# Kernel tuning notes

Hardware: AMD Instinct MI355X
Metric: run time of the kernel (lower is better)

The kernel has to match this reference:

```python
import jax, jax.numpy as jnp
import numpy as np

HIDDEN, HEADS, HDIM = 1024, 8, 64
B, S = 4, 8192
LN_EPS = 1e-6


def setup_inputs() -> dict:
    key = jax.random.key(0)
    ks = jax.random.split(key, 12)
    inner = HEADS * HDIM
    sd = HIDDEN ** -0.5
    return {
        "x": jax.random.normal(ks[0], (B, S, HIDDEN), jnp.float32),
        "Wq": jax.random.normal(ks[1], (HIDDEN, inner), jnp.float32) * sd,
        "bq": jnp.zeros((inner,), jnp.float32),
        "Wk": jax.random.normal(ks[2], (HIDDEN, inner), jnp.float32) * sd,
        "bk": jnp.zeros((inner,), jnp.float32),
        "Wv": jax.random.normal(ks[3], (HIDDEN, inner), jnp.float32) * sd,
        "bv": jnp.zeros((inner,), jnp.float32),
        "Wo": jax.random.normal(ks[4], (inner, HIDDEN), jnp.float32) * (inner ** -0.5),
        "bo": jnp.zeros((HIDDEN,), jnp.float32),
        "alpha": jnp.ones((HEADS, HDIM), jnp.float32),
        "aug_param": jax.random.normal(ks[5], (1, HEADS, HDIM), jnp.float32),
        "ln_scale": jnp.ones((HIDDEN,), jnp.float32),
        "ln_bias": jnp.zeros((HIDDEN,), jnp.float32),
    }


def reference(x, Wq, bq, Wk, bk, Wv, bv, Wo, bo, alpha, aug_param, ln_scale, ln_bias):
    b, s, _ = x.shape
    h, d = alpha.shape
    scale = d ** -0.5
    q = (x @ Wq + bq).reshape(b, s, h, d)
    k = (x @ Wk + bk).reshape(b, s, h, d)
    v = (x @ Wv + bv).reshape(b, s, h, d)
    decay = jax.nn.sigmoid(alpha)  # (h, d)

    def step(state, qkv):
        q_t, k_t, v_t = qkv  # each (b, h, d)
        attn = jax.nn.softmax(jnp.einsum('bhd,bhd->bh', q_t, k_t) * scale, axis=-1)
        new_state = decay * state + (1.0 - decay) * attn[..., None] * v_t
        return new_state, new_state

    qs = jnp.moveaxis(q, 1, 0)  # (s, b, h, d)
    ks_ = jnp.moveaxis(k, 1, 0)
    vs = jnp.moveaxis(v, 1, 0)
    init = jnp.zeros((b, h, d), x.dtype)
    _, states = jax.lax.scan(step, init, (qs, ks_, vs))
    states = jnp.moveaxis(states, 0, 1)  # (b, s, h, d)

    aug = jax.nn.sigmoid(q * aug_param)  # aug_param (1,h,d) broadcasts over (b,s,h,d)
    out = (q * states + aug).reshape(b, s, h * d)
    out = out @ Wo + bo
    mean = jnp.mean(out, axis=-1, keepdims=True)
    var = jnp.var(out, axis=-1, keepdims=True)
    return (out - mean) * jax.lax.rsqrt(var + LN_EPS) * ln_scale + ln_bias
```

## Files before the change

### kernel.cpp

```cpp
#include <hip/hip_runtime.h>
#include <hip/hip_bf16.h>


#define HIDDEN 1024
#define HEADS 8
#define HDIM 64
#define INNER 512
#define BATCH 4
#define SEQ 8192
#define ROWS (BATCH*SEQ)
#define NCHUNK 128
#define CHLEN 64

typedef unsigned short u16;
typedef unsigned int u32;
typedef __attribute__((ext_vector_type(8))) short bf16x8;
typedef __attribute__((ext_vector_type(4))) float f32x4;

__device__ __forceinline__ float b2f(u16 u) { return __uint_as_float(((u32)u) << 16); }
__device__ __forceinline__ u16 f2b(float f) {
  u32 u = __float_as_uint(f);
  u32 r = u + 0x7fffu + ((u >> 16) & 1u);
  return (u16)(r >> 16);
}
__device__ __forceinline__ u32 pack2(float a, float b) {
  return (u32)f2b(a) | ((u32)f2b(b) << 16);
}

#define GLOAD_LDS16(gp, lp)                                                  \
  __builtin_amdgcn_global_load_lds(                                          \
      (const __attribute__((address_space(1))) u32*)(gp),                    \
      (__attribute__((address_space(3))) u32*)(lp), 16, 0, 0)

__global__ __launch_bounds__(256) void prep_xw(
    const float* __restrict__ x, u16* __restrict__ xb,
    const float* __restrict__ Wq, const float* __restrict__ Wk,
    const float* __restrict__ Wv, const float* __restrict__ Wo,
    const float* __restrict__ bq, const float* __restrict__ bk,
    const float* __restrict__ bv,
    u16* __restrict__ Wt, u16* __restrict__ Wot, float* __restrict__ bcat) {
  const int b = blockIdx.x;
  if (b < 16384) {
    size_t i = ((size_t)b * 256 + threadIdx.x) * 8;
    float4 a = *(const float4*)(x + i);
    float4 c = *(const float4*)(x + i + 4);
    uint4 w = {pack2(a.x, a.y), pack2(a.z, a.w), pack2(c.x, c.y), pack2(c.z, c.w)};
    *(uint4*)(xb + i) = w;
  } else {
    const int WELEM = HIDDEN * INNER;
    int idx = (b - 16384) * 256 + threadIdx.x;
    if (idx < 3 * WELEM) {
      int z = idx / WELEM;
      int rem = idx - z * WELEM;
      int n = rem >> 10;
      int k = rem & 1023;
      const float* W = (z == 0) ? Wq : (z == 1) ? Wk : Wv;
      Wt[idx] = f2b(W[k * INNER + n]);
    } else {
      int rem = idx - 3 * WELEM;
      int n = rem >> 9;
      int k = rem & 511;
      Wot[rem] = f2b(Wo[k * HIDDEN + n]);
    }
    if (idx < 3 * INNER) {
      int z = idx >> 9;
      int n = idx & 511;
      bcat[idx] = (z == 0) ? bq[n] : (z == 1) ? bk[n] : bv[n];
    }
  }
}

__global__ __launch_bounds__(256) void prep_w(
    const float* __restrict__ Wq, const float* __restrict__ Wk,
    const float* __restrict__ Wv, const float* __restrict__ Wo,
    const float* __restrict__ bq, const float* __restrict__ bk,
    const float* __restrict__ bv,
    u16* __restrict__ Wt, u16* __restrict__ Wot, float* __restrict__ bcat) {
  const int WELEM = HIDDEN * INNER;
  int idx = blockIdx.x * 256 + threadIdx.x;
  if (idx < 3 * WELEM) {
    int z = idx / WELEM;
    int rem = idx - z * WELEM;
    int n = rem >> 10;
    int k = rem & 1023;
    const float* W = (z == 0) ? Wq : (z == 1) ? Wk : Wv;
    Wt[idx] = f2b(W[k * INNER + n]);
  } else {
    int rem = idx - 3 * WELEM;
    int n = rem >> 9;
    int k = rem & 511;
    Wot[rem] = f2b(Wo[k * HIDDEN + n]);
  }
  if (idx < 3 * INNER) {
    int z = idx >> 9;
    int n = idx & 511;
    bcat[idx] = (z == 0) ? bq[n] : (z == 1) ? bk[n] : bv[n];
  }
}

template <int K, bool SPLIT3>
__global__ __launch_bounds__(512, 2) void gemm_rp(
    const u16* __restrict__ A, const u16* __restrict__ Bt,
    const float* __restrict__ bias,
    void* __restrict__ out0, void* __restrict__ out1, void* __restrict__ out2,
    int nTilesN) {
  constexpr int NT = K / 32;
  __shared__ u16 lds[4][16384];

  const int nwg = gridDim.x;
  const int chunk = nwg >> 3;
  const int bid = blockIdx.x;
  const int lin = (bid & 7) * chunk + (bid >> 3);
  const int nt = lin % nTilesN;
  const int mt = lin / nTilesN;
  const int m0 = mt * 256, n0 = nt * 256;
  const int N = nTilesN * 256;

  const int tid = threadIdx.x;
  const int lane = tid & 63;
  const int w = tid >> 6;
  const int wm = w >> 2;
  const int wn = w & 3;
  const int r16 = lane & 15, kq = lane >> 4;

  const int rt = tid >> 2;
  const int cg = (((tid & 3) << 3)) ^ (((rt >> 1) & 3) << 3);
  const u16* Ag = A + (size_t)(m0 + rt) * K + cg;
  const u16* Bg = Bt + (size_t)(n0 + rt) * K + cg;
  const int ldst = w * 512;

#define STAGE_AB(slot, kt)                                                    \
  {                                                                           \
    GLOAD_LDS16(Ag + (size_t)(kt) * 32, &lds[slot][ldst]);                    \
    GLOAD_LDS16(Ag + (size_t)(kt) * 32 + (size_t)128 * K,                     \
                &lds[slot][4096 + ldst]);                                     \
    GLOAD_LDS16(Bg + (size_t)(kt) * 32, &lds[slot][8192 + ldst]);             \
    GLOAD_LDS16(Bg + (size_t)(kt) * 32 + (size_t)128 * K,                     \
                &lds[slot][12288 + ldst]);                                    \
  }

  const int xk = (kq << 3) ^ (((r16 >> 1) & 3) << 3);
  const int aO = (wm * 128 + r16) * 32 + xk;
  const int bO = 8192 + (wn * 64 + r16) * 32 + xk;

  f32x4 acc[8][4] = {};
  bf16x8 r0_a[8], r0_b[4], r1_a[8], r1_b[4];

#define DSREAD(da, db, slot)                                                   \
  {                                                                            \
    const u16* sl = &lds[slot][0];                                             \
    _Pragma("unroll") for (int i = 0; i < 8; i++)                              \
        da[i] = *(const bf16x8*)&sl[aO + i * 512];                             \
    _Pragma("unroll") for (int j = 0; j < 4; j++)                              \
        db[j] = *(const bf16x8*)&sl[bO + j * 512];                             \
  }

#define MFMA_SET(sa, sb)                                                       \
  {                                                                            \
    __builtin_amdgcn_s_setprio(1);                                             \
    _Pragma("unroll") for (int i = 0; i < 8; i++)                              \
        _Pragma("unroll") for (int j = 0; j < 4; j++)                          \
            acc[i][j] = __builtin_amdgcn_mfma_f32_16x16x32_bf16(               \
                sa[i], sb[j], acc[i][j], 0, 0, 0);                             \
    __builtin_amdgcn_s_setprio(0);                                             \
  }

#define MFMA_RD(sa, sb, da, db, slot)                                          \
  {                                                                            \
    const u16* sl = &lds[slot][0];                                             \
    __builtin_amdgcn_s_setprio(1);                                             \
    _Pragma("unroll") for (int j = 0; j < 4; j++)                              \
        db[j] = *(const bf16x8*)&sl[bO + j * 512];                             \
    _Pragma("unroll") for (int i = 0; i < 8; i++) {                            \
      da[i] = *(const bf16x8*)&sl[aO + i * 512];                               \
      _Pragma("unroll") for (int j = 0; j < 4; j++)                            \
          acc[i][j] = __builtin_amdgcn_mfma_f32_16x16x32_bf16(                 \
              sa[i], sb[j], acc[i][j], 0, 0, 0);                               \
    }                                                                          \
    __builtin_amdgcn_s_setprio(0);                                             \
    __builtin_amdgcn_sched_group_barrier(0x100, 4, 0);        \
    _Pragma("unroll") for (int i = 0; i < 8; i++) {                            \
      __builtin_amdgcn_sched_group_barrier(0x100, 1, 0);      \
      __builtin_amdgcn_sched_group_barrier(0x8, 4, 0);             \
    }                                                                          \
  }

#define SYNCB                                                                  \
  {                                                                            \
    __builtin_amdgcn_sched_barrier(0);                                         \
    __builtin_amdgcn_s_barrier();                                              \
    __builtin_amdgcn_sched_barrier(0);                                         \
  }

#define VM4 asm volatile("s_waitcnt vmcnt(4)" ::: "memory")
#define VM0 asm volatile("s_waitcnt vmcnt(0)" ::: "memory")

  STAGE_AB(0, 0);
  STAGE_AB(1, 1);
  STAGE_AB(2, 2);
  VM4;
  SYNCB;
  DSREAD(r0_a, r0_b, 0);

  for (int t = 0; t + 6 <= NT; t += 2) {
    STAGE_AB((t + 3) & 3, t + 3);
    MFMA_RD(r0_a, r0_b, r1_a, r1_b, (t + 1) & 3);
    VM4;
    SYNCB;
    STAGE_AB((t + 4) & 3, t + 4);
    MFMA_RD(r1_a, r1_b, r0_a, r0_b, (t + 2) & 3);
    VM4;
    SYNCB;
  }
  STAGE_AB((NT - 1) & 3, NT - 1);
  MFMA_RD(r0_a, r0_b, r1_a, r1_b, (NT - 3) & 3);
  VM4;
  SYNCB;
  MFMA_RD(r1_a, r1_b, r0_a, r0_b, (NT - 2) & 3);
  VM0;
  SYNCB;
  MFMA_RD(r0_a, r0_b, r1_a, r1_b, (NT - 1) & 3);
  MFMA_SET(r1_a, r1_b);
  SYNCB;
#undef DSREAD
#undef MFMA_SET
#undef MFMA_RD
#undef SYNCB
#undef VM4
#undef VM0
#undef STAGE_AB

  float* fl = (float*)(&lds[0][0]) + w * 4096;
  const int zsel = SPLIT3 ? ((n0 + wn * 64) >> 9) : 0;
  u16* ob = SPLIT3 ? (u16*)((zsel == 0) ? out0 : (zsel == 1) ? out1 : out2)
                   : (u16*)out0;
  const int OC = SPLIT3 ? INNER : N;
  const int colloc = (lane & 7) * 8;
  const int gcol = (SPLIT3 ? ((n0 + wn * 64) & 511) : (n0 + wn * 64)) + colloc;
  const int lrowr = lane >> 3;
  float bvj[4];
#pragma unroll
  for (int j = 0; j < 4; j++) bvj[j] = bias[n0 + wn * 64 + j * 16 + r16];

#pragma unroll
  for (int pass = 0; pass < 4; ++pass) {
#pragma unroll
    for (int ii = 0; ii < 2; ++ii) {
#pragma unroll
      for (int j = 0; j < 4; ++j) {
#pragma unroll
        for (int q = 0; q < 4; ++q)
          fl[(ii * 16 + kq * 4 + q) * 68 + j * 16 + r16] =
              acc[pass * 2 + ii][j][q] + bvj[j];
      }
    }
#pragma unroll
    for (int inst = 0; inst < 4; ++inst) {
      int lr = inst * 8 + lrowr;
      float4 f0 = *(float4*)&fl[lr * 68 + colloc];
      float4 f1 = *(float4*)&fl[lr * 68 + colloc + 4];
      uint4 wv = {pack2(f0.x, f0.y), pack2(f0.z, f0.w),
                  pack2(f1.x, f1.y), pack2(f1.z, f1.w)};
      size_t grow = (size_t)(m0 + wm * 128 + pass * 32 + lr);
      *(uint4*)&ob[grow * OC + gcol] = wv;
    }
  }
}

template <bool A_BF16>
__global__ __launch_bounds__(256) void gemm128(
    const void* __restrict__ Aany, const u16* __restrict__ BtBase,
    const float* __restrict__ bias0, const float* __restrict__ bias1,
    const float* __restrict__ bias2,
    void* __restrict__ out0, void* __restrict__ out1, void* __restrict__ out2,
    int K) {
  __shared__ u16 As[128 * 32];
  __shared__ u16 Bs[128 * 32];
  const int N = gridDim.x * 128;
  const int z = blockIdx.z;
  const u16* Bt = BtBase + (size_t)z * N * K;
  const float* bias = (z == 0) ? bias0 : (z == 1) ? bias1 : bias2;
  void* Out = (z == 0) ? out0 : (z == 1) ? out1 : out2;
  const int tid = threadIdx.x;
  const int m0 = blockIdx.y * 128;
  const int n0 = blockIdx.x * 128;
  const int lane = tid & 63;
  const int wid = tid >> 6;
  const int wm = wid >> 1, wn = wid & 1;
  const int r16 = lane & 15, kq = lane >> 4;
  const int r = tid >> 1;
  const int half = tid & 1;
  f32x4 acc[4][4] = {};
  for (int k0 = 0; k0 < K; k0 += 32) {
    __syncthreads();
    if (A_BF16) {
      const u16* Ab = (const u16*)Aany;
      const int4* src = (const int4*)(Ab + (size_t)(m0 + r) * K + k0 + half * 16);
      int4 v0 = src[0];
      int4 v1 = src[1];
      *(int4*)&As[r * 32 + half * 16] = v0;
      *(int4*)&As[r * 32 + half * 16 + 8] = v1;
    } else {
      const float* Af = (const float*)Aany;
      const float4* src = (const float4*)(Af + (size_t)(m0 + r) * K + k0 + half * 16);
      float4 f0 = src[0], f1 = src[1], f2 = src[2], f3 = src[3];
      uint4 w0 = {pack2(f0.x, f0.y), pack2(f0.z, f0.w), pack2(f1.x, f1.y), pack2(f1.z, f1.w)};
      uint4 w1 = {pack2(f2.x, f2.y), pack2(f2.z, f2.w), pack2(f3.x, f3.y), pack2(f3.z, f3.w)};
      *(uint4*)&As[r * 32 + half * 16] = w0;
      *(uint4*)&As[r * 32 + half * 16 + 8] = w1;
    }
    {
      const int4* src = (const int4*)(Bt + (size_t)(n0 + r) * K + k0 + half * 16);
      int4 v0 = src[0];
      int4 v1 = src[1];
      *(int4*)&Bs[r * 32 + half * 16] = v0;
      *(int4*)&Bs[r * 32 + half * 16 + 8] = v1;
    }
    __syncthreads();
    bf16x8 a[4], b[4];
#pragma unroll
    for (int i = 0; i < 4; i++)
      a[i] = *(const bf16x8*)&As[(wm * 64 + i * 16 + r16) * 32 + kq * 8];
#pragma unroll
    for (int j = 0; j < 4; j++)
      b[j] = *(const bf16x8*)&Bs[(wn * 64 + j * 16 + r16) * 32 + kq * 8];
#pragma unroll
    for (int i = 0; i < 4; i++)
#pragma unroll
      for (int j = 0; j < 4; j++)
        acc[i][j] = __builtin_amdgcn_mfma_f32_16x16x32_bf16(a[i], b[j], acc[i][j], 0, 0, 0);
  }
#pragma unroll
  for (int j = 0; j < 4; j++) {
    int col = n0 + wn * 64 + j * 16 + r16;
    float bv = bias[col];
#pragma unroll
    for (int i = 0; i < 4; i++) {
#pragma unroll
      for (int q = 0; q < 4; q++) {
        int row = m0 + wm * 64 + i * 16 + kq * 4 + q;
        float v = acc[i][j][q] + bv;
        ((u16*)Out)[(size_t)row * N + col] = f2b(v);
      }
    }
  }
}

__global__ __launch_bounds__(256) void attn_kernel(
    const u16* __restrict__ qb, const u16* __restrict__ kb,
    float* __restrict__ attn) {
  int lane = threadIdx.x & 63;
  int wid = threadIdx.x >> 6;
  size_t t = (size_t)blockIdx.x * 4 + wid;
  int4 qv = *(const int4*)(qb + t * INNER + lane * 8);
  int4 kv = *(const int4*)(kb + t * INNER + lane * 8);
  const u16* qu = (const u16*)&qv;
  const u16* ku = (const u16*)&kv;
  float s = 0.f;
#pragma unroll
  for (int j = 0; j < 8; j++) s += b2f(qu[j]) * b2f(ku[j]);
  s += __shfl_xor(s, 1);
  s += __shfl_xor(s, 2);
  s += __shfl_xor(s, 4);
  s *= 0.125f;
  float mx = s;
  mx = fmaxf(mx, __shfl_xor(mx, 8));
  mx = fmaxf(mx, __shfl_xor(mx, 16));
  mx = fmaxf(mx, __shfl_xor(mx, 32));
  float e = __expf(s - mx);
  float sm = e;
  sm += __shfl_xor(sm, 8);
  sm += __shfl_xor(sm, 16);
  sm += __shfl_xor(sm, 32);
  float a = e / sm;
  if ((lane & 7) == 0) attn[t * HEADS + (lane >> 3)] = a;
}

__global__ __launch_bounds__(512) void scan_phase1(
    const u16* __restrict__ vb, const float* __restrict__ attn,
    const float* __restrict__ alpha, float* __restrict__ ends) {
  int hd = threadIdx.x;
  int h = hd >> 6;
  int c = blockIdx.x, b = blockIdx.y;
  float decay = 1.f / (1.f + __expf(-alpha[hd]));
  float om = 1.f - decay;
  size_t base = (size_t)b * SEQ + (size_t)c * CHLEN;
  float st = 0.f;
#pragma unroll 8
  for (int i = 0; i < CHLEN; i++) {
    size_t t = base + i;
    float a = attn[t * HEADS + h];
    float v = b2f(vb[t * INNER + hd]);
    st = decay * st + om * a * v;
  }
  ends[((size_t)b * NCHUNK + c) * INNER + hd] = st;
}

__global__ __launch_bounds__(512) void scan_phase2(
    const float* __restrict__ ends, const float* __restrict__ alpha,
    float* __restrict__ carries) {
  int hd = threadIdx.x;
  int b = blockIdx.x;
  float decay = 1.f / (1.f + __expf(-alpha[hd]));
  float dL = __powf(decay, (float)CHLEN);
  float carry = 0.f;
#pragma unroll 8
  for (int c = 0; c < NCHUNK; c++) {
    size_t idx = ((size_t)b * NCHUNK + c) * INNER + hd;
    carries[idx] = carry;
    carry = dL * carry + ends[idx];
  }
}

__global__ __launch_bounds__(512) void scan_phase3(
    const u16* __restrict__ qb, const u16* __restrict__ vb,
    const float* __restrict__ attn, const float* __restrict__ alpha,
    const float* __restrict__ augp, const float* __restrict__ carries,
    u16* __restrict__ outpre) {
  int hd = threadIdx.x;
  int h = hd >> 6;
  int c = blockIdx.x, b = blockIdx.y;
  float decay = 1.f / (1.f + __expf(-alpha[hd]));
  float om = 1.f - decay;
  float ap = augp[hd];
  float st = carries[((size_t)b * NCHUNK + c) * INNER + hd];
  size_t base = (size_t)b * SEQ + (size_t)c * CHLEN;
#pragma unroll 4
  for (int i = 0; i < CHLEN; i++) {
    size_t t = base + i;
    float a = attn[t * HEADS + h];
    float v = b2f(vb[t * INNER + hd]);
    st = decay * st + om * a * v;
    float q = b2f(qb[t * INNER + hd]);
    float aug = 1.f / (1.f + __expf(-q * ap));
    outpre[t * INNER + hd] = f2b(q * st + aug);
  }
}

__global__ __launch_bounds__(256) void ln_kernel(
    const u16* __restrict__ outln, float* __restrict__ out,
    const float* __restrict__ lns, const float* __restrict__ lnb) {
  size_t row = blockIdx.x;
  int tid = threadIdx.x;
  uint2 rv = *(const uint2*)(outln + row * HIDDEN + tid * 4);
  const u16* p = (const u16*)&rv;
  float v0 = b2f(p[0]), v1 = b2f(p[1]), v2 = b2f(p[2]), v3 = b2f(p[3]);
  float s = v0 + v1 + v2 + v3;
  float ss = v0 * v0 + v1 * v1 + v2 * v2 + v3 * v3;
#pragma unroll
  for (int m = 1; m < 64; m <<= 1) {
    s += __shfl_xor(s, m);
    ss += __shfl_xor(ss, m);
  }
  __shared__ float sb[4], ssb[4];
  int lane = tid & 63, wid = tid >> 6;
  if (lane == 0) {
    sb[wid] = s;
    ssb[wid] = ss;
  }
  __syncthreads();
  s = sb[0] + sb[1] + sb[2] + sb[3];
  ss = ssb[0] + ssb[1] + ssb[2] + ssb[3];
  float mean = s * (1.f / HIDDEN);
  float var = ss * (1.f / HIDDEN) - mean * mean;
  float rstd = rsqrtf(var + 1e-6f);
  float4 sc = *(const float4*)(lns + tid * 4);
  float4 bi = *(const float4*)(lnb + tid * 4);
  float4 o;
  o.x = (v0 - mean) * rstd * sc.x + bi.x;
  o.y = (v1 - mean) * rstd * sc.y + bi.y;
  o.z = (v2 - mean) * rstd * sc.z + bi.z;
  o.w = (v3 - mean) * rstd * sc.w + bi.w;
  *(float4*)(out + row * HIDDEN + tid * 4) = o;
}

extern "C" void kernel_launch(void* const* d_in, const int* in_sizes, int n_in,
                              void* d_out, int out_size, void* d_ws, size_t ws_size,
                              hipStream_t stream) {
  const float* x = (const float*)d_in[0];
  const float* Wq = (const float*)d_in[1];
  const float* bq = (const float*)d_in[2];
  const float* Wk = (const float*)d_in[3];
  const float* bk = (const float*)d_in[4];
  const float* Wv = (const float*)d_in[5];
  const float* bv = (const float*)d_in[6];
  const float* Wo = (const float*)d_in[7];
  const float* bo = (const float*)d_in[8];
  const float* alpha = (const float*)d_in[9];
  const float* augp = (const float*)d_in[10];
  const float* lns = (const float*)d_in[11];
  const float* lnb = (const float*)d_in[12];

  char* ws = (char*)d_ws;
  const bool fast = ws_size >= 175118336ull;

  if (fast) {
    u16* xb = (u16*)(ws + 0);
    u16* qb = (u16*)(ws + 67108864);
    u16* kb = (u16*)(ws + 100663296);
    u16* vb = (u16*)(ws + 134217728);
    u16* Wt = (u16*)(ws + 167772160);
    u16* Wot = (u16*)(ws + 170917888);
    float* bcat = (float*)(ws + 171966464);
    float* attn = (float*)(ws + 171972608);
    float* ends = (float*)(ws + 173021184);
    float* car = (float*)(ws + 174069760);
    u16* outpre = kb;
    u16* outln = xb;

    prep_xw<<<24576, 256, 0, stream>>>(x, xb, Wq, Wk, Wv, Wo, bq, bk, bv,
                                       Wt, Wot, bcat);

    gemm_rp<HIDDEN, true><<<768, 512, 0, stream>>>(
        xb, Wt, bcat, qb, kb, vb, 6);

    attn_kernel<<<ROWS / 4, 256, 0, stream>>>(qb, kb, attn);
    scan_phase1<<<dim3(NCHUNK, BATCH), 512, 0, stream>>>(vb, attn, alpha, ends);
    scan_phase2<<<BATCH, 512, 0, stream>>>(ends, alpha, car);
    scan_phase3<<<dim3(NCHUNK, BATCH), 512, 0, stream>>>(qb, vb, attn, alpha, augp, car, outpre);

    gemm_rp<INNER, false><<<512, 512, 0, stream>>>(
        outpre, Wot, bo, outln, outln, outln, 4);

    ln_kernel<<<ROWS, 256, 0, stream>>>(outln, (float*)d_out, lns, lnb);
  } else {
    u16* qb = (u16*)(ws + 0);
    u16* vb = (u16*)(ws + 33554432);
    u16* kb = (u16*)(ws + 67108864);
    u16* Wt = (u16*)(ws + 100663296);
    u16* Wot = (u16*)(ws + 103809024);
    float* bcat = (float*)(ws + 104845312);
    float* attn = (float*)(ws + 104857600);
    float* ends = (float*)(ws + 105906176);
    float* car = (float*)(ws + 106954752);
    u16* outpre = kb;
    u16* outln = (u16*)(ws + 0);

    prep_w<<<8192, 256, 0, stream>>>(Wq, Wk, Wv, Wo, bq, bk, bv, Wt, Wot, bcat);
    gemm128<false><<<dim3(4, 256, 3), 256, 0, stream>>>(
        x, Wt, bq, bk, bv, qb, kb, vb, HIDDEN);
    attn_kernel<<<ROWS / 4, 256, 0, stream>>>(qb, kb, attn);
    scan_phase1<<<dim3(NCHUNK, BATCH), 512, 0, stream>>>(vb, attn, alpha, ends);
    scan_phase2<<<BATCH, 512, 0, stream>>>(ends, alpha, car);
    scan_phase3<<<dim3(NCHUNK, BATCH), 512, 0, stream>>>(qb, vb, attn, alpha, augp, car, outpre);
    gemm_rp<INNER, false><<<512, 512, 0, stream>>>(
        outpre, Wot, bo, outln, outln, outln, 4);
    ln_kernel<<<ROWS, 256, 0, stream>>>(outln, (float*)d_out, lns, lnb);
  }
}
```

Measured before the change: 267.3 us.

## Switch GEMM to 32x32x16 MFMA tiles and spread scan phase2 across blocks

The main GEMM now uses the 32x32x16 bf16 MFMA instruction with 4x2 accumulator tiles of 16 floats instead of 8x4 tiles of 16x16x32. This cuts the instruction count and LDS operand reads per FLOP, and the LDS read offsets and the epilogue row mapping are reworked to match. Separately, the serial scan_phase2 now launches 8x4 blocks of 64 threads instead of 4 blocks of 512, spreading the carry propagation over more compute units. The new MFMA layout carries some risk of errors in the swizzle and row mapping, and the epilogue now uses a smaller per-wave LDS stride.

```diff
diff --git a/kernel.cpp b/kernel.cpp
--- a/kernel.cpp
+++ b/kernel.cpp
@@ -16,6 +16,7 @@
 typedef unsigned int u32;
 typedef __attribute__((ext_vector_type(8))) short bf16x8;
 typedef __attribute__((ext_vector_type(4))) float f32x4;
+typedef __attribute__((ext_vector_type(16))) float f32x16;
 
 __device__ __forceinline__ float b2f(u16 u) { return __uint_as_float(((u32)u) << 16); }
 __device__ __forceinline__ u16 f2b(float f) {
@@ -121,7 +122,6 @@
   const int w = tid >> 6;
   const int wm = w >> 2;
   const int wn = w & 3;
-  const int r16 = lane & 15, kq = lane >> 4;
 
   const int rt = tid >> 2;
   const int cg = (((tid & 3) << 3)) ^ (((rt >> 1) & 3) << 3);
@@ -139,29 +139,38 @@
                 &lds[slot][12288 + ldst]);                                    \
   }
 
-  const int xk = (kq << 3) ^ (((r16 >> 1) & 3) << 3);
-  const int aO = (wm * 128 + r16) * 32 + xk;
-  const int bO = 8192 + (wn * 64 + r16) * 32 + xk;
-
-  f32x4 acc[8][4] = {};
+  const int r31 = lane & 31;
+  const int hi8 = (lane >> 5) << 3;
+  const int xr = ((r31 >> 1) & 3) << 3;
+  const int xs0 = hi8 ^ xr;
+  const int xs1 = (16 + hi8) ^ xr;
+  const int aO = (wm * 128 + r31) * 32;
+  const int bO = 8192 + (wn * 64 + r31) * 32;
+
+  f32x16 acc[4][2] = {};
   bf16x8 r0_a[8], r0_b[4], r1_a[8], r1_b[4];
 
 #define DSREAD(da, db, slot)                                                   \
   {                                                                            \
     const u16* sl = &lds[slot][0];                                             \
-    _Pragma("unroll") for (int i = 0; i < 8; i++)                              \
-        da[i] = *(const bf16x8*)&sl[aO + i * 512];                             \
-    _Pragma("unroll") for (int j = 0; j < 4; j++)                              \
-        db[j] = *(const bf16x8*)&sl[bO + j * 512];                             \
+    _Pragma("unroll") for (int it = 0; it < 4; it++) {                         \
+      da[it * 2] = *(const bf16x8*)&sl[aO + it * 1024 + xs0];                  \
+      da[it * 2 + 1] = *(const bf16x8*)&sl[aO + it * 1024 + xs1];              \
+    }                                                                          \
+    _Pragma("unroll") for (int jt = 0; jt < 2; jt++) {                         \
+      db[jt * 2] = *(const bf16x8*)&sl[bO + jt * 1024 + xs0];                  \
+      db[jt * 2 + 1] = *(const bf16x8*)&sl[bO + jt * 1024 + xs1];              \
+    }                                                                          \
   }
 
 #define MFMA_SET(sa, sb)                                                       \
   {                                                                            \
     __builtin_amdgcn_s_setprio(1);                                             \
-    _Pragma("unroll") for (int i = 0; i < 8; i++)                              \
-        _Pragma("unroll") for (int j = 0; j < 4; j++)                          \
-            acc[i][j] = __builtin_amdgcn_mfma_f32_16x16x32_bf16(               \
-                sa[i], sb[j], acc[i][j], 0, 0, 0);                             \
+    _Pragma("unroll") for (int it = 0; it < 4; it++)                           \
+        _Pragma("unroll") for (int jt = 0; jt < 2; jt++)                       \
+            _Pragma("unroll") for (int s = 0; s < 2; s++)                      \
+                acc[it][jt] = __builtin_amdgcn_mfma_f32_32x32x16_bf16(         \
+                    sa[it * 2 + s], sb[jt * 2 + s], acc[it][jt], 0, 0, 0);     \
     __builtin_amdgcn_s_setprio(0);                                             \
   }
 
@@ -169,18 +178,22 @@
   {                                                                            \
     const u16* sl = &lds[slot][0];                                             \
     __builtin_amdgcn_s_setprio(1);                                             \
-    _Pragma("unroll") for (int j = 0; j < 4; j++)                              \
-        db[j] = *(const bf16x8*)&sl[bO + j * 512];                             \
-    _Pragma("unroll") for (int i = 0; i < 8; i++) {                            \
-      da[i] = *(const bf16x8*)&sl[aO + i * 512];                               \
-      _Pragma("unroll") for (int j = 0; j < 4; j++)                            \
-          acc[i][j] = __builtin_amdgcn_mfma_f32_16x16x32_bf16(                 \
-              sa[i], sb[j], acc[i][j], 0, 0, 0);                               \
+    _Pragma("unroll") for (int jt = 0; jt < 2; jt++) {                         \
+      db[jt * 2] = *(const bf16x8*)&sl[bO + jt * 1024 + xs0];                  \
+      db[jt * 2 + 1] = *(const bf16x8*)&sl[bO + jt * 1024 + xs1];              \
+    }                                                                          \
+    _Pragma("unroll") for (int it = 0; it < 4; it++) {                         \
+      da[it * 2] = *(const bf16x8*)&sl[aO + it * 1024 + xs0];                  \
+      da[it * 2 + 1] = *(const bf16x8*)&sl[aO + it * 1024 + xs1];              \
+      _Pragma("unroll") for (int jt = 0; jt < 2; jt++)                         \
+          _Pragma("unroll") for (int s = 0; s < 2; s++)                        \
+              acc[it][jt] = __builtin_amdgcn_mfma_f32_32x32x16_bf16(           \
+                  sa[it * 2 + s], sb[jt * 2 + s], acc[it][jt], 0, 0, 0);       \
     }                                                                          \
     __builtin_amdgcn_s_setprio(0);                                             \
     __builtin_amdgcn_sched_group_barrier(0x100, 4, 0);        \
-    _Pragma("unroll") for (int i = 0; i < 8; i++) {                            \
-      __builtin_amdgcn_sched_group_barrier(0x100, 1, 0);      \
+    _Pragma("unroll") for (int it = 0; it < 4; it++) {                         \
+      __builtin_amdgcn_sched_group_barrier(0x100, 2, 0);      \
       __builtin_amdgcn_sched_group_barrier(0x8, 4, 0);             \
     }                                                                          \
   }
@@ -230,7 +243,7 @@
 #undef VM0
 #undef STAGE_AB
 
-  float* fl = (float*)(&lds[0][0]) + w * 4096;
+  float* fl = (float*)(&lds[0][0]) + w * 2176;
   const int zsel = SPLIT3 ? ((n0 + wn * 64) >> 9) : 0;
   u16* ob = SPLIT3 ? (u16*)((zsel == 0) ? out0 : (zsel == 1) ? out1 : out2)
                    : (u16*)out0;
@@ -238,20 +251,19 @@
   const int colloc = (lane & 7) * 8;
   const int gcol = (SPLIT3 ? ((n0 + wn * 64) & 511) : (n0 + wn * 64)) + colloc;
   const int lrowr = lane >> 3;
-  float bvj[4];
-#pragma unroll
-  for (int j = 0; j < 4; j++) bvj[j] = bias[n0 + wn * 64 + j * 16 + r16];
-
-#pragma unroll
-  for (int pass = 0; pass < 4; ++pass) {
-#pragma unroll
-    for (int ii = 0; ii < 2; ++ii) {
-#pragma unroll
-      for (int j = 0; j < 4; ++j) {
-#pragma unroll
-        for (int q = 0; q < 4; ++q)
-          fl[(ii * 16 + kq * 4 + q) * 68 + j * 16 + r16] =
-              acc[pass * 2 + ii][j][q] + bvj[j];
+  const int hi4 = (lane >> 5) << 2;
+  float bvj[2];
+#pragma unroll
+  for (int jt = 0; jt < 2; jt++) bvj[jt] = bias[n0 + wn * 64 + jt * 32 + r31];
+
+#pragma unroll
+  for (int it = 0; it < 4; ++it) {
+#pragma unroll
+    for (int jt = 0; jt < 2; ++jt) {
+#pragma unroll
+      for (int r = 0; r < 16; ++r) {
+        int lrow = (r & 3) + ((r >> 2) << 3) + hi4;
+        fl[lrow * 68 + jt * 32 + r31] = acc[it][jt][r] + bvj[jt];
       }
     }
 #pragma unroll
@@ -261,7 +273,7 @@
       float4 f1 = *(float4*)&fl[lr * 68 + colloc + 4];
       uint4 wv = {pack2(f0.x, f0.y), pack2(f0.z, f0.w),
                   pack2(f1.x, f1.y), pack2(f1.z, f1.w)};
-      size_t grow = (size_t)(m0 + wm * 128 + pass * 32 + lr);
+      size_t grow = (size_t)(m0 + wm * 128 + it * 32 + lr);
       *(uint4*)&ob[grow * OC + gcol] = wv;
     }
   }
@@ -396,11 +408,11 @@
   ends[((size_t)b * NCHUNK + c) * INNER + hd] = st;
 }
 
-__global__ __launch_bounds__(512) void scan_phase2(
+__global__ __launch_bounds__(64) void scan_phase2(
     const float* __restrict__ ends, const float* __restrict__ alpha,
     float* __restrict__ carries) {
-  int hd = threadIdx.x;
-  int b = blockIdx.x;
+  int hd = blockIdx.x * 64 + threadIdx.x;
+  int b = blockIdx.y;
   float decay = 1.f / (1.f + __expf(-alpha[hd]));
   float dL = __powf(decay, (float)CHLEN);
   float carry = 0.f;
@@ -516,7 +528,7 @@
 
     attn_kernel<<<ROWS / 4, 256, 0, stream>>>(qb, kb, attn);
     scan_phase1<<<dim3(NCHUNK, BATCH), 512, 0, stream>>>(vb, attn, alpha, ends);
-    scan_phase2<<<BATCH, 512, 0, stream>>>(ends, alpha, car);
+    scan_phase2<<<dim3(8, BATCH), 64, 0, stream>>>(ends, alpha, car);
     scan_phase3<<<dim3(NCHUNK, BATCH), 512, 0, stream>>>(qb, vb, attn, alpha, augp, car, outpre);
 
     gemm_rp<INNER, false><<<512, 512, 0, stream>>>(
@@ -541,7 +553,7 @@
         x, Wt, bq, bk, bv, qb, kb, vb, HIDDEN);
     attn_kernel<<<ROWS / 4, 256, 0, stream>>>(qb, kb, attn);
     scan_phase1<<<dim3(NCHUNK, BATCH), 512, 0, stream>>>(vb, attn, alpha, ends);
-    scan_phase2<<<BATCH, 512, 0, stream>>>(ends, alpha, car);
+    scan_phase2<<<dim3(8, BATCH), 64, 0, stream>>>(ends, alpha, car);
     scan_phase3<<<dim3(NCHUNK, BATCH), 512, 0, stream>>>(qb, vb, attn, alpha, augp, car, outpre);
     gemm_rp<INNER, false><<<512, 512, 0, stream>>>(
         outpre, Wot, bo, outln, outln, outln, 4);
```

New measurement: 283.7 us. 1.06x slower.
